# Optimization experiments

Measured on AMD Instinct MI355X. Metric: run time of the kernel, lower is better.

The kernel has to match this reference:

```python
import jax, jax.numpy as jnp
import numpy as np

X_DIM = Y_DIM = 512      # render resolution (create_coords x_dim, y_dim)
X_MAX = Y_MAX = 512      # grid extents (== x_mode, y_mode)
Z_DIM = 64
Z_MIN, Z_MAX = 0.0, 1.0
FEATS = 32
BATCH = 8


def _make_coords(x_dim, y_dim, x_max, y_max):
    # Faithful replica of G_Tensor3D.create_coords (incl. half_dx used for ys start).
    half_dx, half_dy = 0.5 / x_dim, 0.5 / y_dim
    xs = np.linspace(half_dx, 1 - half_dx, x_dim, dtype=np.float32)
    ys = np.linspace(half_dx, 1 - half_dy, y_dim, dtype=np.float32)
    xv, yv = np.meshgrid(xs, ys, indexing='ij')
    xy = np.stack((yv.ravel(), xv.ravel()), axis=1)              # [N, 2]
    s = xy * np.array([x_max, y_max], dtype=np.float32)          # scaled coords
    idx = s.astype(np.int64)
    x0 = np.clip(idx[:, 0], 0, x_max - 1)
    y0 = np.clip(idx[:, 1], 0, y_max - 1)
    x1 = np.minimum(x0 + 1, x_max - 1)
    y1 = np.minimum(y0 + 1, y_max - 1)
    lerp = (s - idx.astype(np.float32)).astype(np.float32)       # [N, 2]
    return x0.astype(np.int32), y0.astype(np.int32), x1.astype(np.int32), y1.astype(np.int32), lerp


def setup_inputs() -> dict:
    key = jax.random.key(0)
    kz, kd, kzd, k1, k2, k3, kb1, kb2, kb3 = jax.random.split(key, 9)
    x0, y0, x1, y1, lerp = _make_coords(X_DIM, Y_DIM, X_MAX, Y_MAX)
    return {
        "z": jax.random.uniform(kz, (BATCH,), dtype=jnp.float32, minval=Z_MIN, maxval=Z_MAX),
        "data": 0.0002 * jax.random.normal(kd, (X_MAX, Y_MAX, FEATS), dtype=jnp.float32),
        "z_data": jax.random.normal(kzd, (Z_DIM, FEATS), dtype=jnp.float32),
        "lerp_weights": jnp.asarray(lerp),
        "x0": jnp.asarray(x0), "y0": jnp.asarray(y0),
        "x1": jnp.asarray(x1), "y1": jnp.asarray(y1),
        "W1": 0.1 * jax.random.normal(k1, (FEATS, 32), dtype=jnp.float32),
        "b1": 0.1 * jax.random.normal(kb1, (32,), dtype=jnp.float32),
        "W2": 0.1 * jax.random.normal(k2, (32, 32), dtype=jnp.float32),
        "b2": 0.1 * jax.random.normal(kb2, (32,), dtype=jnp.float32),
        "W3": 0.1 * jax.random.normal(k3, (32, 1), dtype=jnp.float32),
        "b3": 0.1 * jax.random.normal(kb3, (1,), dtype=jnp.float32),
    }


def reference(z, data, z_data, lerp_weights, x0, y0, x1, y1, W1, b1, W2, b2, W3, b3):
    b = z.shape[0]
    # --- z interpolation (torch .long() truncates; z >= 0 here) ---
    zn = (Z_DIM - 1) * (z - Z_MIN) / (Z_MAX - Z_MIN)
    z0i = jnp.clip(zn.astype(jnp.int32), 0, Z_DIM - 1)
    z1i = jnp.minimum(z0i + 1, Z_DIM - 1)
    zl = (zn - jnp.trunc(zn))[:, None]                           # [b, 1]
    z_feat = z_data[z0i] * (1.0 - zl) + z_data[z1i] * zl         # [b, F]
    # --- bilinear spatial gather (note data indexed [y, x] as in source) ---
    wx = lerp_weights[:, 0:1]
    wy = lerp_weights[:, 1:2]
    xy_feat = (data[y0, x0] * (1.0 - wx) * (1.0 - wy)
               + data[y0, x1] * wx * (1.0 - wy)
               + data[y1, x0] * (1.0 - wx) * wy
               + data[y1, x1] * wx * wy)                          # [N, F]
    # --- outer broadcast product + tiny MLP ---
    feat = xy_feat[None, :, :] * z_feat[:, None, :]              # [b, N, F]
    h = jax.nn.relu(feat @ W1 + b1)
    h = jax.nn.relu(h @ W2 + b2)
    out = h @ W3 + b3                                            # [b, N, 1]
    return out.reshape(b, 1, X_DIM, Y_DIM)
```

## Files before the change

### kernel.cpp

```cpp
#include <hip/hip_runtime.h>


typedef float f32x4 __attribute__((ext_vector_type(4)));
typedef short bf16x8 __attribute__((ext_vector_type(8)));

constexpr int NPIX = 512 * 512;
constexpr int PPB  = 64;

union FragU { unsigned int u[4]; uint4 v; bf16x8 s; };

__device__ __forceinline__ unsigned int pack_top16(float e0, float e1) {
    return __builtin_amdgcn_perm(__float_as_uint(e1), __float_as_uint(e0), 0x07060302u);
}
__device__ __forceinline__ float trunc_bf16(float x) {
    return __uint_as_float(__float_as_uint(x) & 0xFFFF0000u);
}

__global__ __launch_bounds__(256, 1) void field_mlp_mfma5(
    const float* __restrict__ z,
    const float* __restrict__ data,
    const float* __restrict__ z_data,
    const float* __restrict__ lerp_w,
    const int* __restrict__ x0a, const int* __restrict__ y0a,
    const int* __restrict__ x1a, const int* __restrict__ y1a,
    const float* __restrict__ W1, const float* __restrict__ b1,
    const float* __restrict__ W2, const float* __restrict__ b2,
    const float* __restrict__ W3, const float* __restrict__ b3,
    float* __restrict__ out)
{
    __shared__ float f_T[PPB][36];
    __shared__ float zf_lds[8][36];
    __shared__ float bias_lds[2][36];
    __shared__ float w3_lds[36];
    __shared__ __align__(16) unsigned int wt_lds[4][32][20];

    const int tid = threadIdx.x;

    {
        const int b = tid >> 5, i = tid & 31;
        const float zn = 63.0f * z[b];
        int z0 = (int)zn; z0 = max(0, min(z0, 63));
        const int z1i = min(z0 + 1, 63);
        const float zl = zn - truncf(zn);
        zf_lds[b][i] = z_data[z0 * 32 + i] * (1.0f - zl) + z_data[z1i * 32 + i] * zl;
    }
    if (tid < 32) {
        bias_lds[0][tid] = b1[tid];
        bias_lds[1][tid] = b2[tid];
        w3_lds[tid]      = W3[tid];
    }
#pragma unroll
    for (int u = 0; u < 2; ++u) {
        const int unit = tid + u * 256;
        const int pxl = unit >> 3, ch = unit & 7;
        const int p = blockIdx.x * PPB + pxl;
        const int ix0 = x0a[p], iy0 = y0a[p], ix1 = x1a[p], iy1 = y1a[p];
        const float2 w2 = *(const float2*)(lerp_w + 2 * p);
        const float wx = w2.x, wy = w2.y;
        const float w00 = (1.0f - wx) * (1.0f - wy);
        const float w01 = wx * (1.0f - wy);
        const float w10 = (1.0f - wx) * wy;
        const float w11 = wx * wy;
        const f32x4* base = (const f32x4*)data;
        const f32x4 c00 = base[(iy0 * 512 + ix0) * 8 + ch];
        const f32x4 c01 = base[(iy0 * 512 + ix1) * 8 + ch];
        const f32x4 c10 = base[(iy1 * 512 + ix0) * 8 + ch];
        const f32x4 c11 = base[(iy1 * 512 + ix1) * 8 + ch];
        const f32x4 v = c00 * w00 + c01 * w01 + c10 * w10 + c11 * w11;
        *(f32x4*)&f_T[pxl][ch * 4] = v;
    }
    {
        const int n = tid & 31, kc = (tid >> 5) * 4, kw = (tid >> 5) * 2;
#pragma unroll
        for (int m = 0; m < 2; ++m) {
            const float* Wm = m ? W2 : W1;
            const float x0 = Wm[(kc + 0) * 32 + n];
            const float x1 = Wm[(kc + 1) * 32 + n];
            const float x2 = Wm[(kc + 2) * 32 + n];
            const float x3 = Wm[(kc + 3) * 32 + n];
            wt_lds[2 * m][n][kw]     = pack_top16(x0, x1);
            wt_lds[2 * m][n][kw + 1] = pack_top16(x2, x3);
            wt_lds[2 * m + 1][n][kw]     = pack_top16(x0 - trunc_bf16(x0), x1 - trunc_bf16(x1));
            wt_lds[2 * m + 1][n][kw + 1] = pack_top16(x2 - trunc_bf16(x2), x3 - trunc_bf16(x3));
        }
    }
    __syncthreads();

    const int l  = tid & 63, w = tid >> 6;
    const int lg = l >> 4,  lr = l & 15;
    const int srow = ((lr >> 2) << 3) + (lr & 3);

    FragU W1f[2][2], W2f[2][2];
#pragma unroll
    for (int t = 0; t < 2; ++t) {
        W1f[t][0].v = *(const uint4*)&wt_lds[0][srow + 4 * t][lg * 4];
        W1f[t][1].v = *(const uint4*)&wt_lds[1][srow + 4 * t][lg * 4];
        W2f[t][0].v = *(const uint4*)&wt_lds[2][t * 16 + lr][lg * 4];
        W2f[t][1].v = *(const uint4*)&wt_lds[3][t * 16 + lr][lg * 4];
    }
    f32x4 zva[2], zvb[2], b1v[2], b2v[2], w3v[2];
#pragma unroll
    for (int bb = 0; bb < 2; ++bb) {
        zva[bb] = *(const f32x4*)&zf_lds[2 * w + bb][lg * 8];
        zvb[bb] = *(const f32x4*)&zf_lds[2 * w + bb][lg * 8 + 4];
    }
#pragma unroll
    for (int t = 0; t < 2; ++t) {
        b1v[t] = *(const f32x4*)&bias_lds[0][8 * lg + 4 * t];
        b2v[t] = *(const f32x4*)&bias_lds[1][t * 16 + 4 * lg];
        w3v[t] = *(const f32x4*)&w3_lds[t * 16 + 4 * lg];
    }
    const float b3s = b3[0];
    const f32x4 vzero = {0.0f, 0.0f, 0.0f, 0.0f};
    float* const outp = out + blockIdx.x * PPB;

#pragma unroll
    for (int pxg = 0; pxg < 4; ++pxg) {
        const int px = pxg * 16 + lr;
        const f32x4 ff0 = *(const f32x4*)&f_T[px][lg * 8];
        const f32x4 ff1 = *(const f32x4*)&f_T[px][lg * 8 + 4];
#pragma unroll
        for (int bb = 0; bb < 2; ++bb) {
            const f32x4 ea = ff0 * zva[bb];
            const f32x4 eb = ff1 * zvb[bb];
            FragU Eh;
            Eh.u[0] = pack_top16(ea[0], ea[1]);
            Eh.u[1] = pack_top16(ea[2], ea[3]);
            Eh.u[2] = pack_top16(eb[0], eb[1]);
            Eh.u[3] = pack_top16(eb[2], eb[3]);
            f32x4 hv[2];
#pragma unroll
            for (int t = 0; t < 2; ++t) {
                f32x4 a = __builtin_amdgcn_mfma_f32_16x16x32_bf16(W1f[t][1].s, Eh.s, vzero, 0, 0, 0);
                a = __builtin_amdgcn_mfma_f32_16x16x32_bf16(W1f[t][0].s, Eh.s, a, 0, 0, 0);
                a = a + b1v[t];
#pragma unroll
                for (int r = 0; r < 4; ++r) a[r] = fmaxf(a[r], 0.0f);
                hv[t] = a;
            }
            FragU Hh, Hl;
            Hh.u[0] = pack_top16(hv[0][0], hv[0][1]);
            Hh.u[1] = pack_top16(hv[0][2], hv[0][3]);
            Hh.u[2] = pack_top16(hv[1][0], hv[1][1]);
            Hh.u[3] = pack_top16(hv[1][2], hv[1][3]);
            f32x4 hl0 = hv[0], hl1 = hv[1];
#pragma unroll
            for (int r = 0; r < 4; ++r) {
                hl0[r] -= trunc_bf16(hv[0][r]);
                hl1[r] -= trunc_bf16(hv[1][r]);
            }
            Hl.u[0] = pack_top16(hl0[0], hl0[1]);
            Hl.u[1] = pack_top16(hl0[2], hl0[3]);
            Hl.u[2] = pack_top16(hl1[0], hl1[1]);
            Hl.u[3] = pack_top16(hl1[2], hl1[3]);
            float o = 0.0f;
#pragma unroll
            for (int t = 0; t < 2; ++t) {
                f32x4 a = __builtin_amdgcn_mfma_f32_16x16x32_bf16(W2f[t][0].s, Hl.s, vzero, 0, 0, 0);
                a = __builtin_amdgcn_mfma_f32_16x16x32_bf16(W2f[t][1].s, Hh.s, a, 0, 0, 0);
                a = __builtin_amdgcn_mfma_f32_16x16x32_bf16(W2f[t][0].s, Hh.s, a, 0, 0, 0);
                a = a + b2v[t];
#pragma unroll
                for (int r = 0; r < 4; ++r)
                    o = fmaf(fmaxf(a[r], 0.0f), w3v[t][r], o);
            }
            o += __shfl_xor(o, 16);
            o += __shfl_xor(o, 32);
            o += b3s;
            if (l < 16)
                __builtin_nontemporal_store(o, outp + (2 * w + bb) * NPIX + px);
        }
    }
}

extern "C" void kernel_launch(void* const* d_in, const int* in_sizes, int n_in,
                              void* d_out, int out_size, void* d_ws, size_t ws_size,
                              hipStream_t stream) {
    const float* zp      = (const float*)d_in[0];
    const float* data    = (const float*)d_in[1];
    const float* z_data  = (const float*)d_in[2];
    const float* lerp_w  = (const float*)d_in[3];
    const int*   x0      = (const int*)d_in[4];
    const int*   y0      = (const int*)d_in[5];
    const int*   x1      = (const int*)d_in[6];
    const int*   y1      = (const int*)d_in[7];
    const float* W1      = (const float*)d_in[8];
    const float* b1      = (const float*)d_in[9];
    const float* W2      = (const float*)d_in[10];
    const float* b2      = (const float*)d_in[11];
    const float* W3      = (const float*)d_in[12];
    const float* b3      = (const float*)d_in[13];
    float* out = (float*)d_out;

    dim3 grid(NPIX / PPB);
    dim3 block(256);
    hipLaunchKernelGGL(field_mlp_mfma5, grid, block, 0, stream,
                       zp, data, z_data, lerp_w, x0, y0, x1, y1,
                       W1, b1, W2, b2, W3, b3, out);
}
```

Measured before the change: 129.6 us.

## Fuse bilinear gather into MFMA loop, fold biases into accumulator init

Removes the separate LDS staging pass for bilinearly interpolated features. Each lane now gathers its own pixel's corner data inside the per-pixel-group loop. Bias vectors become the initial MFMA accumulators instead of separate adds. Launch bounds are relaxed and the pixel loop is no longer unrolled. As a result, each of the 4 waves redundantly gathers the same pixels, which increases global and L2 traffic in exchange for removing a barrier and the LDS round trip.

```diff
diff --git a/kernel.cpp b/kernel.cpp
--- a/kernel.cpp
+++ b/kernel.cpp
@@ -16,7 +16,7 @@
     return __uint_as_float(__float_as_uint(x) & 0xFFFF0000u);
 }
 
-__global__ __launch_bounds__(256, 1) void field_mlp_mfma5(
+__global__ __launch_bounds__(256) void field_mlp_mfma6(
     const float* __restrict__ z,
     const float* __restrict__ data,
     const float* __restrict__ z_data,
@@ -28,7 +28,6 @@
     const float* __restrict__ W3, const float* __restrict__ b3,
     float* __restrict__ out)
 {
-    __shared__ float f_T[PPB][36];
     __shared__ float zf_lds[8][36];
     __shared__ float bias_lds[2][36];
     __shared__ float w3_lds[36];
@@ -48,26 +47,6 @@
         bias_lds[0][tid] = b1[tid];
         bias_lds[1][tid] = b2[tid];
         w3_lds[tid]      = W3[tid];
-    }
-#pragma unroll
-    for (int u = 0; u < 2; ++u) {
-        const int unit = tid + u * 256;
-        const int pxl = unit >> 3, ch = unit & 7;
-        const int p = blockIdx.x * PPB + pxl;
-        const int ix0 = x0a[p], iy0 = y0a[p], ix1 = x1a[p], iy1 = y1a[p];
-        const float2 w2 = *(const float2*)(lerp_w + 2 * p);
-        const float wx = w2.x, wy = w2.y;
-        const float w00 = (1.0f - wx) * (1.0f - wy);
-        const float w01 = wx * (1.0f - wy);
-        const float w10 = (1.0f - wx) * wy;
-        const float w11 = wx * wy;
-        const f32x4* base = (const f32x4*)data;
-        const f32x4 c00 = base[(iy0 * 512 + ix0) * 8 + ch];
-        const f32x4 c01 = base[(iy0 * 512 + ix1) * 8 + ch];
-        const f32x4 c10 = base[(iy1 * 512 + ix0) * 8 + ch];
-        const f32x4 c11 = base[(iy1 * 512 + ix1) * 8 + ch];
-        const f32x4 v = c00 * w00 + c01 * w01 + c10 * w10 + c11 * w11;
-        *(f32x4*)&f_T[pxl][ch * 4] = v;
     }
     {
         const int n = tid & 31, kc = (tid >> 5) * 4, kw = (tid >> 5) * 2;
@@ -111,14 +90,28 @@
         w3v[t] = *(const f32x4*)&w3_lds[t * 16 + 4 * lg];
     }
     const float b3s = b3[0];
-    const f32x4 vzero = {0.0f, 0.0f, 0.0f, 0.0f};
-    float* const outp = out + blockIdx.x * PPB;
+    const int pbase = blockIdx.x * PPB;
+    float* const outp = out + pbase;
+    const f32x4* const dbase = (const f32x4*)data + 2 * lg;
 
-#pragma unroll
+#pragma unroll 1
     for (int pxg = 0; pxg < 4; ++pxg) {
         const int px = pxg * 16 + lr;
-        const f32x4 ff0 = *(const f32x4*)&f_T[px][lg * 8];
-        const f32x4 ff1 = *(const f32x4*)&f_T[px][lg * 8 + 4];
+        const int p  = pbase + px;
+        const int ix0 = x0a[p], iy0 = y0a[p], ix1 = x1a[p], iy1 = y1a[p];
+        const float2 w2 = *(const float2*)(lerp_w + 2 * p);
+        const float wx = w2.x, wy = w2.y;
+        const float w00 = (1.0f - wx) * (1.0f - wy);
+        const float w01 = wx * (1.0f - wy);
+        const float w10 = (1.0f - wx) * wy;
+        const float w11 = wx * wy;
+        const f32x4* c00 = dbase + (iy0 * 512 + ix0) * 8;
+        const f32x4* c01 = dbase + (iy0 * 512 + ix1) * 8;
+        const f32x4* c10 = dbase + (iy1 * 512 + ix0) * 8;
+        const f32x4* c11 = dbase + (iy1 * 512 + ix1) * 8;
+        const f32x4 ff0 = c00[0] * w00 + c01[0] * w01 + c10[0] * w10 + c11[0] * w11;
+        const f32x4 ff1 = c00[1] * w00 + c01[1] * w01 + c10[1] * w10 + c11[1] * w11;
+
 #pragma unroll
         for (int bb = 0; bb < 2; ++bb) {
             const f32x4 ea = ff0 * zva[bb];
@@ -131,9 +124,8 @@
             f32x4 hv[2];
 #pragma unroll
             for (int t = 0; t < 2; ++t) {
-                f32x4 a = __builtin_amdgcn_mfma_f32_16x16x32_bf16(W1f[t][1].s, Eh.s, vzero, 0, 0, 0);
+                f32x4 a = __builtin_amdgcn_mfma_f32_16x16x32_bf16(W1f[t][1].s, Eh.s, b1v[t], 0, 0, 0);
                 a = __builtin_amdgcn_mfma_f32_16x16x32_bf16(W1f[t][0].s, Eh.s, a, 0, 0, 0);
-                a = a + b1v[t];
 #pragma unroll
                 for (int r = 0; r < 4; ++r) a[r] = fmaxf(a[r], 0.0f);
                 hv[t] = a;
@@ -156,10 +148,9 @@
             float o = 0.0f;
 #pragma unroll
             for (int t = 0; t < 2; ++t) {
-                f32x4 a = __builtin_amdgcn_mfma_f32_16x16x32_bf16(W2f[t][0].s, Hl.s, vzero, 0, 0, 0);
+                f32x4 a = __builtin_amdgcn_mfma_f32_16x16x32_bf16(W2f[t][0].s, Hl.s, b2v[t], 0, 0, 0);
                 a = __builtin_amdgcn_mfma_f32_16x16x32_bf16(W2f[t][1].s, Hh.s, a, 0, 0, 0);
                 a = __builtin_amdgcn_mfma_f32_16x16x32_bf16(W2f[t][0].s, Hh.s, a, 0, 0, 0);
-                a = a + b2v[t];
 #pragma unroll
                 for (int r = 0; r < 4; ++r)
                     o = fmaf(fmaxf(a[r], 0.0f), w3v[t][r], o);
@@ -194,7 +185,7 @@
 
     dim3 grid(NPIX / PPB);
     dim3 block(256);
-    hipLaunchKernelGGL(field_mlp_mfma5, grid, block, 0, stream,
+    hipLaunchKernelGGL(field_mlp_mfma6, grid, block, 0, stream,
                        zp, data, z_data, lerp_w, x0, y0, x1, y1,
                        W1, b1, W2, b2, W3, b3, out);
 }
```

Result: slower. 163.2 us (+25.9%).
